# Performance work log

Hardware: AMD Instinct MI355X
Metric: run time of the kernel (lower is better)

Reference implementation:

```python
import jax, jax.numpy as jnp
import numpy as np

EPS = 1e-16
LOG_2PI = float(np.log(2.0 * np.pi))
DUMMY = -2.0 * float(np.log(10.0))  # dummy component logit / log-prob


def setup_inputs() -> dict:
    key = jax.random.key(0)
    k1, k2, k3, k4, k5 = jax.random.split(key, 5)
    B, N, V, D = 32, 1024, 512, 4
    x = jax.random.normal(k1, (B, N, D), dtype=jnp.float32)
    votes = jax.random.normal(k2, (B, V, D), dtype=jnp.float32)
    # positive stds in [0.1, 1.0)
    scales = jax.random.uniform(k3, (B, V), dtype=jnp.float32) * 0.9 + 0.1
    vote_presence_prob = jax.random.uniform(k4, (B, V), dtype=jnp.float32)
    presence = jax.random.uniform(k5, (B, N), dtype=jnp.float32)
    return {"x": x, "votes": votes, "scales": scales,
            "vote_presence_prob": vote_presence_prob,
            "presence": presence, "n_votes": 16}


def reference(x, votes, scales, vote_presence_prob, presence, n_votes):
    B, N, D = x.shape
    V = votes.shape[1]
    # Broadcast Normal log-prob: x [B,N,1,D] vs votes [B,1,V,D], scale [B,1,V,1]
    sig = scales[:, None, :, None]
    z = (x[:, :, None, :] - votes[:, None, :, :]) / sig
    lp_per_dim = -0.5 * z * z - jnp.log(sig) - 0.5 * LOG_2PI
    vote_log_prob = jnp.sum(lp_per_dim, axis=-1)                       # [B,N,V]
    vote_log_prob = jnp.concatenate(
        [vote_log_prob, jnp.full((B, N, 1), DUMMY, vote_log_prob.dtype)], axis=2)  # [B,N,V+1]

    mixing_logits = jnp.log(vote_presence_prob + EPS)                  # safe_log, [B,V]
    mixing_logits = jnp.concatenate(
        [mixing_logits, jnp.full((B, 1), DUMMY, mixing_logits.dtype)], axis=1)     # [B,V+1]
    mixing_log_prob = jax.nn.log_softmax(mixing_logits, axis=1)        # [B,V+1]

    posterior = mixing_log_prob[:, None, :] + vote_log_prob            # [B,N,V+1]
    mixture_lp_per_comp = jax.scipy.special.logsumexp(posterior, axis=2)  # [B,N]
    mixture_lp_per_comp = mixture_lp_per_comp * presence
    log_prob = jnp.sum(mixture_lp_per_comp)                            # scalar

    winning_vote_idx = jnp.argmax(posterior[:, :, :-1], axis=2)        # [B,N]
    winner = jnp.take_along_axis(votes, winning_vote_idx[:, :, None], axis=1)  # [B,N,D]
    winner_pres = jnp.take_along_axis(vote_presence_prob, winning_vote_idx, axis=1)  # [B,N]
    vote_presence = (mixing_logits[:, :-1] > mixing_logits[:, -1:]).astype(jnp.float32)  # [B,V]
    is_from_capsule = winning_vote_idx // n_votes                      # [B,N]
    posterior_mixing_probs = jax.nn.softmax(posterior, axis=-1)[..., :-1]  # [B,N,V]

    return (log_prob, vote_presence, winner, winner_pres, is_from_capsule,
            mixing_logits, mixing_log_prob, jnp.zeros_like(winner),
            jnp.zeros_like(winner_pres), posterior_mixing_probs)
```

## Files before the change

kernel.cpp:

```cpp
#include <hip/hip_runtime.h>

typedef float v2f __attribute__((ext_vector_type(2)));

#define FEPS 1e-16f
#define LOG_2PI 1.8378770664093453f
#define DUMMYV -4.605170185988091f
#define LOG2E 1.4426950408889634f
#define LN2 0.6931471805599453f

constexpr int B = 32, N = 1024, V = 512;
constexpr int ROWS_PER_BLOCK = 32;
constexpr int GRID_X = N / ROWS_PER_BLOCK;

constexpr long long OFF_LOGPROB    = 0;
constexpr long long OFF_VOTEPRES   = 1;
constexpr long long OFF_WINNER     = OFF_VOTEPRES + (long long)B * V;
constexpr long long OFF_WINNERPRES = OFF_WINNER + (long long)B * N * 4;
constexpr long long OFF_ISFROM     = OFF_WINNERPRES + (long long)B * N;
constexpr long long OFF_MLOGITS    = OFF_ISFROM + (long long)B * N;
constexpr long long OFF_MLOGPROB   = OFF_MLOGITS + (long long)B * (V + 1);
constexpr long long OFF_ZW         = OFF_MLOGPROB + (long long)B * (V + 1);
constexpr long long OFF_ZWP       = OFF_ZW + (long long)B * N * 4;
constexpr long long OFF_PMP        = OFF_ZWP + (long long)B * N;

__device__ __forceinline__ float fexp2(float x) {
#if __has_builtin(__builtin_amdgcn_exp2f)
    return __builtin_amdgcn_exp2f(x);
#else
    return __expf(x * LN2);
#endif
}
__device__ __forceinline__ float frcp(float x) {
#if __has_builtin(__builtin_amdgcn_rcpf)
    return __builtin_amdgcn_rcpf(x);
#else
    return 1.0f / x;
#endif
}

template<int RN> __device__ __forceinline__ float dppRorF(float x) {
    return __int_as_float(__builtin_amdgcn_update_dpp(
        0, __float_as_int(x), 0x120 | RN, 0xF, 0xF, false));
}
template<int RN> __device__ __forceinline__ int dppRorI(int x) {
    return __builtin_amdgcn_update_dpp(0, x, 0x120 | RN, 0xF, 0xF, false);
}
__device__ __forceinline__ float swz16F(float x) {
    return __int_as_float(__builtin_amdgcn_ds_swizzle(__float_as_int(x), 0x401F));
}
__device__ __forceinline__ int swz16I(int x) {
    return __builtin_amdgcn_ds_swizzle(x, 0x401F);
}

#if __has_builtin(__builtin_amdgcn_permlane32_swap)
__device__ __forceinline__ float maxSwap32(float x) {
    auto r = __builtin_amdgcn_permlane32_swap(__float_as_uint(x), __float_as_uint(x), false, false);
    return fmaxf(__uint_as_float(r[0]), __uint_as_float(r[1]));
}
__device__ __forceinline__ float sumSwap32(float x) {
    auto r = __builtin_amdgcn_permlane32_swap(__float_as_uint(x), __float_as_uint(x), false, false);
    return __uint_as_float(r[0]) + __uint_as_float(r[1]);
}
__device__ __forceinline__ int minSwap32(int x) {
    auto r = __builtin_amdgcn_permlane32_swap((unsigned)x, (unsigned)x, false, false);
    int a = (int)r[0], b = (int)r[1];
    return a < b ? a : b;
}
#else
__device__ __forceinline__ float maxSwap32(float x) { return fmaxf(x, __shfl_xor(x, 32)); }
__device__ __forceinline__ float sumSwap32(float x) { return x + __shfl_xor(x, 32); }
__device__ __forceinline__ int   minSwap32(int x)   { int o = __shfl_xor(x, 32); return o < x ? o : x; }
#endif

__device__ __forceinline__ float waveMaxF(float m) {
    m = fmaxf(m, dppRorF<1>(m));
    m = fmaxf(m, dppRorF<2>(m));
    m = fmaxf(m, dppRorF<4>(m));
    m = fmaxf(m, dppRorF<8>(m));
    m = fmaxf(m, swz16F(m));
    return maxSwap32(m);
}
__device__ __forceinline__ float waveSumF(float s) {
    s += dppRorF<1>(s);
    s += dppRorF<2>(s);
    s += dppRorF<4>(s);
    s += dppRorF<8>(s);
    s += swz16F(s);
    return sumSwap32(s);
}
__device__ __forceinline__ int waveMinI(int v) {
    int o;
    o = dppRorI<1>(v); v = o < v ? o : v;
    o = dppRorI<2>(v); v = o < v ? o : v;
    o = dppRorI<4>(v); v = o < v ? o : v;
    o = dppRorI<8>(v); v = o < v ? o : v;
    o = swz16I(v);     v = o < v ? o : v;
    return minSwap32(v);
}

__global__ __launch_bounds__(256) void k_fused(const float* __restrict__ x,
                                               const float* __restrict__ votes,
                                               const float* __restrict__ scales,
                                               const float* __restrict__ vpp,
                                               const float* __restrict__ presence,
                                               const int* __restrict__ nvp,
                                               float* __restrict__ out,
                                               float* __restrict__ ws) {
    __shared__ float s_c2[512], s_hk[512], s_ax[512], s_ay[512], s_az[512], s_aw[512];
    __shared__ float s_m[4], s_s[4], s_part[4];

    const int b = blockIdx.y, t = threadIdx.x, w = t >> 6, lane = t & 63;
    const long long bV = (long long)b * V;
    const float4* votes4 = reinterpret_cast<const float4*>(votes) + bV;

    const int va = w * 128 + lane, vb = va + 64;
    float4 v4a = votes4[va], v4b = votes4[vb];
    float sva = scales[bV + va], svb = scales[bV + vb];
    float lga = __logf(vpp[bV + va] + FEPS);
    float lgb = __logf(vpp[bV + vb] + FEPS);

    float mm = waveMaxF(fmaxf(lga, lgb));
    if (lane == 0) s_m[w] = mm;
    __syncthreads();
    float M = fmaxf(fmaxf(fmaxf(s_m[0], s_m[1]), fmaxf(s_m[2], s_m[3])), DUMMYV);
    float ss = waveSumF(__expf(lga - M) + __expf(lgb - M));
    if (lane == 0) s_s[w] = ss;
    __syncthreads();
    float S = s_s[0] + s_s[1] + s_s[2] + s_s[3] + __expf(DUMMYV - M);
    float lse = M + __logf(S);
    float dummy_post = DUMMYV + (DUMMYV - lse);

    {
        float4 vv = v4a;
        float inv = frcp(sva);
        float hh = 0.5f * inv * inv;
        float c = lga - 4.0f * __logf(sva) - 2.0f * LOG_2PI - lse;
        float v2 = vv.x * vv.x + vv.y * vv.y + vv.z * vv.z + vv.w * vv.w;
        int idx = ((va >> 7) << 7) + ((va & 63) << 1) + ((va >> 6) & 1);
        float g = 2.0f * hh * LOG2E;
        s_c2[idx] = (c - hh * v2 - dummy_post) * LOG2E;
        s_hk[idx] = -hh * LOG2E;
        s_ax[idx] = g * vv.x; s_ay[idx] = g * vv.y;
        s_az[idx] = g * vv.z; s_aw[idx] = g * vv.w;
    }
    {
        float4 vv = v4b;
        float inv = frcp(svb);
        float hh = 0.5f * inv * inv;
        float c = lgb - 4.0f * __logf(svb) - 2.0f * LOG_2PI - lse;
        float v2 = vv.x * vv.x + vv.y * vv.y + vv.z * vv.z + vv.w * vv.w;
        int idx = ((vb >> 7) << 7) + ((vb & 63) << 1) + ((vb >> 6) & 1);
        float g = 2.0f * hh * LOG2E;
        s_c2[idx] = (c - hh * v2 - dummy_post) * LOG2E;
        s_hk[idx] = -hh * LOG2E;
        s_ax[idx] = g * vv.x; s_ay[idx] = g * vv.y;
        s_az[idx] = g * vv.z; s_aw[idx] = g * vv.w;
    }

    if (blockIdx.x == 0) {
        long long mb = (long long)b * (V + 1);
        out[OFF_MLOGITS  + mb + va] = lga;
        out[OFF_MLOGITS  + mb + vb] = lgb;
        out[OFF_MLOGPROB + mb + va] = lga - lse;
        out[OFF_MLOGPROB + mb + vb] = lgb - lse;
        out[OFF_VOTEPRES + bV + va] = (lga > DUMMYV) ? 1.0f : 0.0f;
        out[OFF_VOTEPRES + bV + vb] = (lgb > DUMMYV) ? 1.0f : 0.0f;
        if (t == 0) {
            out[OFF_MLOGITS  + mb + V] = DUMMYV;
            out[OFF_MLOGPROB + mb + V] = DUMMYV - lse;
        }
    }
    __syncthreads();

    v2f c2[4], hk[4], hvx[4], hvy[4], hvz[4], hvw[4];
    #pragma unroll
    for (int i = 0; i < 4; ++i) {
        int o = i * 128 + lane * 2;
        c2[i]  = *reinterpret_cast<const v2f*>(&s_c2[o]);
        hk[i]  = *reinterpret_cast<const v2f*>(&s_hk[o]);
        hvx[i] = *reinterpret_cast<const v2f*>(&s_ax[o]);
        hvy[i] = *reinterpret_cast<const v2f*>(&s_ay[o]);
        hvz[i] = *reinterpret_cast<const v2f*>(&s_az[o]);
        hvw[i] = *reinterpret_cast<const v2f*>(&s_aw[o]);
    }

    const float4* x4 = reinterpret_cast<const float4*>(x) + (long long)b * N;
    int nv = nvp[0];
    float acc = 0.f;

    #pragma unroll 2
    for (int iter = 0; iter < ROWS_PER_BLOCK / 4; ++iter) {
        int n = blockIdx.x * ROWS_PER_BLOCK + iter * 4 + w;
        long long bn = (long long)b * N + n;
        float4 xv = x4[n];
        float px2 = xv.x * xv.x + xv.y * xv.y + xv.z * xv.z + xv.w * xv.w;
        v2f P2; P2.x = px2;  P2.y = px2;
        v2f Xx; Xx.x = xv.x; Xx.y = xv.x;
        v2f Xy; Xy.x = xv.y; Xy.y = xv.y;
        v2f Xz; Xz.x = xv.z; Xz.y = xv.z;
        v2f Xw; Xw.x = xv.w; Xw.y = xv.w;

        float p2s[8];
        #pragma unroll
        for (int i = 0; i < 4; ++i) {
            v2f tt = c2[i];
            tt += hk[i]  * P2;
            tt += hvx[i] * Xx;
            tt += hvy[i] * Xy;
            tt += hvz[i] * Xz;
            tt += hvw[i] * Xw;
            p2s[2 * i]     = tt.x;
            p2s[2 * i + 1] = tt.y;
        }

        float t1 = fmaxf(fmaxf(p2s[0], p2s[1]), p2s[2]);
        float t2 = fmaxf(fmaxf(p2s[3], p2s[4]), p2s[5]);
        float t3 = fmaxf(fmaxf(p2s[6], p2s[7]), t1);
        float Mrow = waveMaxF(fmaxf(t2, t3));

        int cand = 0x7fffffff;
        #pragma unroll
        for (int k = 0; k < 8; ++k)
            if (p2s[k] == Mrow && (k * 64 + lane) < cand) cand = k * 64 + lane;
        int bi = waveMinI(cand);

        float e[8];
        float se = 0.f;
        #pragma unroll
        for (int k = 0; k < 8; ++k) { e[k] = fexp2(p2s[k]); se += e[k]; }
        se = waveSumF(se);
        float total = se + 1.0f;
        float rt = frcp(total);

        long long pb = OFF_PMP + bn * (long long)V;
        #pragma unroll
        for (int k = 0; k < 8; ++k)
            out[pb + k * 64 + lane] = e[k] * rt;

        if (lane == 0) {
            acc += (dummy_post + LN2 * __log2f(total)) * presence[bn];
            float4 wv = votes4[bi];
            out[OFF_WINNER + bn * 4 + 0] = wv.x;
            out[OFF_WINNER + bn * 4 + 1] = wv.y;
            out[OFF_WINNER + bn * 4 + 2] = wv.z;
            out[OFF_WINNER + bn * 4 + 3] = wv.w;
            out[OFF_WINNERPRES + bn]     = vpp[bV + bi];
            out[OFF_ISFROM + bn]         = (float)((nv == 16) ? (bi >> 4) : (bi / nv));
        }
        if (lane == 1) {
            out[OFF_ZW + bn * 4 + 0] = 0.f;
            out[OFF_ZW + bn * 4 + 1] = 0.f;
            out[OFF_ZW + bn * 4 + 2] = 0.f;
            out[OFF_ZW + bn * 4 + 3] = 0.f;
            out[OFF_ZWP + bn]        = 0.f;
        }
    }

    if (lane == 0) s_part[w] = acc;
    __syncthreads();
    if (t == 0)
        ws[(long long)b * gridDim.x + blockIdx.x] =
            s_part[0] + s_part[1] + s_part[2] + s_part[3];
}

__global__ __launch_bounds__(256) void k_reduce(const float* __restrict__ ws,
                                                float* __restrict__ out, int count) {
    __shared__ float sred[256];
    int t = threadIdx.x;
    float s = 0.f;
    for (int i = t; i < count; i += 256) s += ws[i];
    sred[t] = s;
    __syncthreads();
    for (int o = 128; o > 0; o >>= 1) {
        if (t < o) sred[t] += sred[t + o];
        __syncthreads();
    }
    if (t == 0) out[OFF_LOGPROB] = sred[0];
}

extern "C" void kernel_launch(void* const* d_in, const int* in_sizes, int n_in,
                              void* d_out, int out_size, void* d_ws, size_t ws_size,
                              hipStream_t stream) {
    const float* x        = (const float*)d_in[0];
    const float* votes    = (const float*)d_in[1];
    const float* scales   = (const float*)d_in[2];
    const float* vpp      = (const float*)d_in[3];
    const float* presence = (const float*)d_in[4];
    const int*   nv       = (const int*)d_in[5];
    float* out = (float*)d_out;
    float* ws  = (float*)d_ws;

    dim3 g(GRID_X, B);
    k_fused<<<g, 256, 0, stream>>>(x, votes, scales, vpp, presence, nv, out, ws);
    k_reduce<<<1, 256, 0, stream>>>(ws, out, GRID_X * B);
}
```

Before: 26.53 us.

## Vectorize posterior stores with alignment-shifted layout and replace reduce kernel with atomics

Reorders the per-vote coefficients in shared memory with a one-element shift so each lane handles four consecutive votes. This lets the posterior probability rows, which start at an odd float offset, be written with aligned 128-bit stores instead of scalar stores. The last lane handles the wraparound elements specially. The second reduction kernel is dropped in favour of a memset plus a per-block atomicAdd into the log-prob scalar, which removes a launch but makes the summation order nondeterministic.

```diff
diff --git a/kernel.cpp b/kernel.cpp
--- a/kernel.cpp
+++ b/kernel.cpp
@@ -1,6 +1,7 @@
 #include <hip/hip_runtime.h>
 
 typedef float v2f __attribute__((ext_vector_type(2)));
+typedef float v4f __attribute__((ext_vector_type(4)));
 
 #define FEPS 1e-16f
 #define LOG_2PI 1.8378770664093453f
@@ -20,7 +21,7 @@
 constexpr long long OFF_MLOGITS    = OFF_ISFROM + (long long)B * N;
 constexpr long long OFF_MLOGPROB   = OFF_MLOGITS + (long long)B * (V + 1);
 constexpr long long OFF_ZW         = OFF_MLOGPROB + (long long)B * (V + 1);
-constexpr long long OFF_ZWP       = OFF_ZW + (long long)B * N * 4;
+constexpr long long OFF_ZWP        = OFF_ZW + (long long)B * N * 4;
 constexpr long long OFF_PMP        = OFF_ZWP + (long long)B * N;
 
 __device__ __forceinline__ float fexp2(float x) {
@@ -106,7 +107,7 @@
                                                const int* __restrict__ nvp,
                                                float* __restrict__ out,
                                                float* __restrict__ ws) {
-    __shared__ float s_c2[512], s_hk[512], s_ax[512], s_ay[512], s_az[512], s_aw[512];
+    __shared__ float s_c2[513], s_hk[513], s_ax[513], s_ay[513], s_az[513], s_aw[513];
     __shared__ float s_m[4], s_s[4], s_part[4];
 
     const int b = blockIdx.y, t = threadIdx.x, w = t >> 6, lane = t & 63;
@@ -136,12 +137,11 @@
         float hh = 0.5f * inv * inv;
         float c = lga - 4.0f * __logf(sva) - 2.0f * LOG_2PI - lse;
         float v2 = vv.x * vv.x + vv.y * vv.y + vv.z * vv.z + vv.w * vv.w;
-        int idx = ((va >> 7) << 7) + ((va & 63) << 1) + ((va >> 6) & 1);
         float g = 2.0f * hh * LOG2E;
-        s_c2[idx] = (c - hh * v2 - dummy_post) * LOG2E;
-        s_hk[idx] = -hh * LOG2E;
-        s_ax[idx] = g * vv.x; s_ay[idx] = g * vv.y;
-        s_az[idx] = g * vv.z; s_aw[idx] = g * vv.w;
+        s_c2[va + 1] = (c - hh * v2 - dummy_post) * LOG2E;
+        s_hk[va + 1] = -hh * LOG2E;
+        s_ax[va + 1] = g * vv.x; s_ay[va + 1] = g * vv.y;
+        s_az[va + 1] = g * vv.z; s_aw[va + 1] = g * vv.w;
     }
     {
         float4 vv = v4b;
@@ -149,12 +149,11 @@
         float hh = 0.5f * inv * inv;
         float c = lgb - 4.0f * __logf(svb) - 2.0f * LOG_2PI - lse;
         float v2 = vv.x * vv.x + vv.y * vv.y + vv.z * vv.z + vv.w * vv.w;
-        int idx = ((vb >> 7) << 7) + ((vb & 63) << 1) + ((vb >> 6) & 1);
         float g = 2.0f * hh * LOG2E;
-        s_c2[idx] = (c - hh * v2 - dummy_post) * LOG2E;
-        s_hk[idx] = -hh * LOG2E;
-        s_ax[idx] = g * vv.x; s_ay[idx] = g * vv.y;
-        s_az[idx] = g * vv.z; s_aw[idx] = g * vv.w;
+        s_c2[vb + 1] = (c - hh * v2 - dummy_post) * LOG2E;
+        s_hk[vb + 1] = -hh * LOG2E;
+        s_ax[vb + 1] = g * vv.x; s_ay[vb + 1] = g * vv.y;
+        s_az[vb + 1] = g * vv.z; s_aw[vb + 1] = g * vv.w;
     }
 
     if (blockIdx.x == 0) {
@@ -172,16 +171,40 @@
     }
     __syncthreads();
 
-    v2f c2[4], hk[4], hvx[4], hvy[4], hvz[4], hvw[4];
+    v4f cA, kA, xA, yA, zA, wA, cB, kB, xB, yB, zB, wB;
+    {
+        int oA = 4 + 4 * lane;
+        cA = *reinterpret_cast<const v4f*>(&s_c2[oA]);
+        kA = *reinterpret_cast<const v4f*>(&s_hk[oA]);
+        xA = *reinterpret_cast<const v4f*>(&s_ax[oA]);
+        yA = *reinterpret_cast<const v4f*>(&s_ay[oA]);
+        zA = *reinterpret_cast<const v4f*>(&s_az[oA]);
+        wA = *reinterpret_cast<const v4f*>(&s_aw[oA]);
+        if (lane < 63) {
+            int oB = 260 + 4 * lane;
+            cB = *reinterpret_cast<const v4f*>(&s_c2[oB]);
+            kB = *reinterpret_cast<const v4f*>(&s_hk[oB]);
+            xB = *reinterpret_cast<const v4f*>(&s_ax[oB]);
+            yB = *reinterpret_cast<const v4f*>(&s_ay[oB]);
+            zB = *reinterpret_cast<const v4f*>(&s_az[oB]);
+            wB = *reinterpret_cast<const v4f*>(&s_aw[oB]);
+        } else {
+            cB.x = s_c2[512]; cB.y = s_c2[1]; cB.z = s_c2[2]; cB.w = s_c2[3];
+            kB.x = s_hk[512]; kB.y = s_hk[1]; kB.z = s_hk[2]; kB.w = s_hk[3];
+            xB.x = s_ax[512]; xB.y = s_ax[1]; xB.z = s_ax[2]; xB.w = s_ax[3];
+            yB.x = s_ay[512]; yB.y = s_ay[1]; yB.z = s_ay[2]; yB.w = s_ay[3];
+            zB.x = s_az[512]; zB.y = s_az[1]; zB.z = s_az[2]; zB.w = s_az[3];
+            wB.x = s_aw[512]; wB.y = s_aw[1]; wB.z = s_aw[2]; wB.w = s_aw[3];
+        }
+    }
+    int vidx[8];
     #pragma unroll
-    for (int i = 0; i < 4; ++i) {
-        int o = i * 128 + lane * 2;
-        c2[i]  = *reinterpret_cast<const v2f*>(&s_c2[o]);
-        hk[i]  = *reinterpret_cast<const v2f*>(&s_hk[o]);
-        hvx[i] = *reinterpret_cast<const v2f*>(&s_ax[o]);
-        hvy[i] = *reinterpret_cast<const v2f*>(&s_ay[o]);
-        hvz[i] = *reinterpret_cast<const v2f*>(&s_az[o]);
-        hvw[i] = *reinterpret_cast<const v2f*>(&s_aw[o]);
+    for (int j = 0; j < 4; ++j) vidx[j] = 3 + 4 * lane + j;
+    if (lane < 63) {
+        #pragma unroll
+        for (int j = 0; j < 4; ++j) vidx[4 + j] = 259 + 4 * lane + j;
+    } else {
+        vidx[4] = 511; vidx[5] = 0; vidx[6] = 1; vidx[7] = 2;
     }
 
     const float4* x4 = reinterpret_cast<const float4*>(x) + (long long)b * N;
@@ -194,48 +217,50 @@
         long long bn = (long long)b * N + n;
         float4 xv = x4[n];
         float px2 = xv.x * xv.x + xv.y * xv.y + xv.z * xv.z + xv.w * xv.w;
-        v2f P2; P2.x = px2;  P2.y = px2;
-        v2f Xx; Xx.x = xv.x; Xx.y = xv.x;
-        v2f Xy; Xy.x = xv.y; Xy.y = xv.y;
-        v2f Xz; Xz.x = xv.z; Xz.y = xv.z;
-        v2f Xw; Xw.x = xv.w; Xw.y = xv.w;
-
-        float p2s[8];
-        #pragma unroll
-        for (int i = 0; i < 4; ++i) {
-            v2f tt = c2[i];
-            tt += hk[i]  * P2;
-            tt += hvx[i] * Xx;
-            tt += hvy[i] * Xy;
-            tt += hvz[i] * Xz;
-            tt += hvw[i] * Xw;
-            p2s[2 * i]     = tt.x;
-            p2s[2 * i + 1] = tt.y;
-        }
-
-        float t1 = fmaxf(fmaxf(p2s[0], p2s[1]), p2s[2]);
-        float t2 = fmaxf(fmaxf(p2s[3], p2s[4]), p2s[5]);
-        float t3 = fmaxf(fmaxf(p2s[6], p2s[7]), t1);
-        float Mrow = waveMaxF(fmaxf(t2, t3));
+        v4f P2 = {px2, px2, px2, px2};
+        v4f Xx = {xv.x, xv.x, xv.x, xv.x};
+        v4f Xy = {xv.y, xv.y, xv.y, xv.y};
+        v4f Xz = {xv.z, xv.z, xv.z, xv.z};
+        v4f Xw = {xv.w, xv.w, xv.w, xv.w};
+
+        v4f pA = cA + kA * P2 + xA * Xx + yA * Xy + zA * Xz + wA * Xw;
+        v4f pB = cB + kB * P2 + xB * Xx + yB * Xy + zB * Xz + wB * Xw;
+
+        v4f m4 = __builtin_elementwise_max(pA, pB);
+        float m_in = fmaxf(fmaxf(m4.x, m4.y), fmaxf(m4.z, m4.w));
+        float Mrow = waveMaxF(m_in);
 
         int cand = 0x7fffffff;
-        #pragma unroll
-        for (int k = 0; k < 8; ++k)
-            if (p2s[k] == Mrow && (k * 64 + lane) < cand) cand = k * 64 + lane;
+        if (pA.x == Mrow) cand = min(cand, vidx[0]);
+        if (pA.y == Mrow) cand = min(cand, vidx[1]);
+        if (pA.z == Mrow) cand = min(cand, vidx[2]);
+        if (pA.w == Mrow) cand = min(cand, vidx[3]);
+        if (pB.x == Mrow) cand = min(cand, vidx[4]);
+        if (pB.y == Mrow) cand = min(cand, vidx[5]);
+        if (pB.z == Mrow) cand = min(cand, vidx[6]);
+        if (pB.w == Mrow) cand = min(cand, vidx[7]);
         int bi = waveMinI(cand);
 
-        float e[8];
-        float se = 0.f;
-        #pragma unroll
-        for (int k = 0; k < 8; ++k) { e[k] = fexp2(p2s[k]); se += e[k]; }
-        se = waveSumF(se);
+        v4f eA, eB;
+        eA.x = fexp2(pA.x); eA.y = fexp2(pA.y); eA.z = fexp2(pA.z); eA.w = fexp2(pA.w);
+        eB.x = fexp2(pB.x); eB.y = fexp2(pB.y); eB.z = fexp2(pB.z); eB.w = fexp2(pB.w);
+        v4f e8 = eA + eB;
+        float se = waveSumF((e8.x + e8.y) + (e8.z + e8.w));
         float total = se + 1.0f;
         float rt = frcp(total);
-
-        long long pb = OFF_PMP + bn * (long long)V;
-        #pragma unroll
-        for (int k = 0; k < 8; ++k)
-            out[pb + k * 64 + lane] = e[k] * rt;
+        v4f rtv = {rt, rt, rt, rt};
+
+        float* rp = out + OFF_PMP + bn * (long long)V;
+        v4f qa = eA * rtv, qb = eB * rtv;
+        *reinterpret_cast<v4f*>(rp + 3 + 4 * lane) = qa;
+        if (lane < 63) {
+            *reinterpret_cast<v4f*>(rp + 259 + 4 * lane) = qb;
+        } else {
+            rp[511] = qb.x;
+            rp[0]   = qb.y;
+            v2f ez = {qb.z, qb.w};
+            *reinterpret_cast<v2f*>(rp + 1) = ez;
+        }
 
         if (lane == 0) {
             acc += (dummy_post + LN2 * __log2f(total)) * presence[bn];
@@ -259,23 +284,8 @@
     if (lane == 0) s_part[w] = acc;
     __syncthreads();
     if (t == 0)
-        ws[(long long)b * gridDim.x + blockIdx.x] =
-            s_part[0] + s_part[1] + s_part[2] + s_part[3];
-}
-
-__global__ __launch_bounds__(256) void k_reduce(const float* __restrict__ ws,
-                                                float* __restrict__ out, int count) {
-    __shared__ float sred[256];
-    int t = threadIdx.x;
-    float s = 0.f;
-    for (int i = t; i < count; i += 256) s += ws[i];
-    sred[t] = s;
-    __syncthreads();
-    for (int o = 128; o > 0; o >>= 1) {
-        if (t < o) sred[t] += sred[t + o];
-        __syncthreads();
-    }
-    if (t == 0) out[OFF_LOGPROB] = sred[0];
+        atomicAdd(out + OFF_LOGPROB,
+                  s_part[0] + s_part[1] + s_part[2] + s_part[3]);
 }
 
 extern "C" void kernel_launch(void* const* d_in, const int* in_sizes, int n_in,
@@ -289,8 +299,10 @@
     const int*   nv       = (const int*)d_in[5];
     float* out = (float*)d_out;
     float* ws  = (float*)d_ws;
+    (void)ws;
+
+    hipMemsetAsync((void*)(out + OFF_LOGPROB), 0, sizeof(float), stream);
 
     dim3 g(GRID_X, B);
     k_fused<<<g, 256, 0, stream>>>(x, votes, scales, vpp, presence, nv, out, ws);
-    k_reduce<<<1, 256, 0, stream>>>(ws, out, GRID_X * B);
-}
+}
```

After: 35.03 us. 1.32x slower.
